# Optimization experiments

Measured on AMD Instinct MI355X. Metric: run time of the kernel, lower is better.

## Reference

```python
import jax, jax.numpy as jnp
import numpy as np

N = 40000      # input points
M = 40000      # output points
E = 500000     # flat neighbor edges (ragged flattened)
F = 32         # input feature channels
C = 64         # output channels
K = 15         # kernel points
EXTENT = 0.6


def _make_kernel_points(k, radius):
    # Deterministic stand-in for load_kernels(): first point fixed at center,
    # remaining points spread inside a ball of the given radius.
    rng = np.random.RandomState(0)
    pts = rng.randn(k, 3).astype(np.float32)
    pts /= np.linalg.norm(pts, axis=1, keepdims=True) + 1e-9
    scale = rng.rand(k, 1).astype(np.float32) ** (1.0 / 3.0)
    pts = pts * scale * radius
    pts[0] = 0.0  # fixed='center'
    return jnp.asarray(pts)


def setup_inputs() -> dict:
    key = jax.random.key(0)
    ks = jax.random.split(key, 6)
    points = jax.random.uniform(ks[0], (N, 3), dtype=jnp.float32)
    features = jax.random.normal(ks[1], (N, F), dtype=jnp.float32)
    output_points = jax.random.uniform(ks[2], (M, 3), dtype=jnp.float32)
    neighbor_indices = jax.random.randint(ks[3], (E,), 0, N, dtype=jnp.int32)
    segment_ids = jnp.sort(jax.random.randint(ks[4], (E,), 0, M, dtype=jnp.int32))
    k_points = _make_kernel_points(K, 1.5 * EXTENT)          # [K,3] constant
    k_values = jax.random.normal(ks[5], (K, F, C), dtype=jnp.float32) * 0.05
    return {
        "points": points,
        "features": features,
        "output_points": output_points,
        "neighbor_indices": neighbor_indices,
        "segment_ids": segment_ids,
        "k_points": k_points,
        "k_values": k_values,
    }


def reference(points, features, output_points, neighbor_indices, segment_ids,
              k_points, k_values):
    # Gather neighbor coords/features and recenter around each output point.
    rel = points[neighbor_indices] - output_points[segment_ids]      # [E,3]
    nbr_feat = features[neighbor_indices]                            # [E,F]

    # Per-kernel-point squared distances and linear influence weights.
    diff = rel[:, None, :] - k_points[None, :, :]                    # [E,K,3]
    sq_dist = jnp.sum(diff * diff, axis=-1)                          # [E,K]
    w = jnp.maximum(1.0 - jnp.sqrt(sq_dist) / EXTENT, 0.0)           # [E,K]

    # Weighted features and ragged segment-sum per output point.
    weighted = w[:, :, None] * nbr_feat[:, None, :]                  # [E,K,F]
    agg = jax.ops.segment_sum(weighted, segment_ids, num_segments=M,
                              indices_are_sorted=True)               # [M,K,F]

    # Batched matmul over kernel points, then sum over kernel points.
    out = jnp.einsum('mkf,kfc->mc', agg, k_values)                   # [M,C]
    return out
```

## Files before the change

kernel.cpp:

```cpp
#include <hip/hip_runtime.h>

typedef __attribute__((ext_vector_type(8))) short bf16x8;
typedef __attribute__((ext_vector_type(8))) _Float16 f16x8;
typedef __attribute__((ext_vector_type(4))) float f32x4;
typedef __attribute__((ext_vector_type(4))) _Float16 f16x4;

#define NPTS   40000
#define MOUT   40000
#define EDG    500000
#define FIN    32
#define COUT   64
#define KP     15
#define KFDIM  (KP * FIN)
#define EXTENT 0.6f

#define FEAT_BLKS  (NPTS * FIN / 1024)
#define PTS_BLKS   ((NPTS + 255) / 256)
#define ROW_BLKS   ((EDG + 255) / 256)
#define PRE_BLKS   (FEAT_BLKS + PTS_BLKS + ROW_BLKS)

__device__ __forceinline__ short f2bf(float x) {
    union { float f; unsigned u; } v; v.f = x;
    unsigned r = (v.u + 0x7fffu + ((v.u >> 16) & 1u)) >> 16;
    return (short)r;
}

__global__ __launch_bounds__(256) void preprocess_all(
    const float* __restrict__ features, _Float16* __restrict__ feat_h,
    const float* __restrict__ pts, float4* __restrict__ p4,
    const int* __restrict__ seg_ids, int* __restrict__ row_start)
{
    const int bid = blockIdx.x;
    if (bid < FEAT_BLKS) {
        const int i = (bid * 256 + threadIdx.x) * 4;
        const float4 v = *(const float4*)(features + i);
        feat_h[i + 0] = (_Float16)v.x;
        feat_h[i + 1] = (_Float16)v.y;
        feat_h[i + 2] = (_Float16)v.z;
        feat_h[i + 3] = (_Float16)v.w;
    } else if (bid < FEAT_BLKS + PTS_BLKS) {
        const int i = (bid - FEAT_BLKS) * 256 + threadIdx.x;
        if (i < NPTS) {
            const float* p = pts + 3 * i;
            p4[i] = make_float4(p[0], p[1], p[2], 0.f);
        }
    } else {
        const int e = (bid - FEAT_BLKS - PTS_BLKS) * 256 + threadIdx.x;
        if (e >= EDG) return;
        const int cur  = seg_ids[e];
        const int prev = (e == 0) ? -1 : seg_ids[e - 1];
        for (int m = prev + 1; m <= cur; ++m) row_start[m] = e;
        if (e == EDG - 1)
            for (int m = cur + 1; m <= MOUT; ++m) row_start[m] = EDG;
    }
}

__global__ __launch_bounds__(256, 8) void kpconv_agg_mfma16(
    const float4* __restrict__ points4,
    const _Float16* __restrict__ feat_h,
    const float* __restrict__ output_points,
    const int*   __restrict__ nbr_idx,
    const int*   __restrict__ row_start,
    const float* __restrict__ k_points,
    _Float16* __restrict__ agg_g)
{
    const int tid  = threadIdx.x;
    const int wave = tid >> 6;
    const int lane = tid & 63;
    const int quad = lane >> 4;
    const int l16  = lane & 15;

    const int m = blockIdx.x * 4 + wave;
    const int e0 = row_start[m], e1 = row_start[m + 1];

    const float ox = output_points[m * 3 + 0];
    const float oy = output_points[m * 3 + 1];
    const float oz = output_points[m * 3 + 2];

    const int myk = l16 < KP ? l16 : 0;
    const float kpx = k_points[myk * 3 + 0];
    const float kpy = k_points[myk * 3 + 1];
    const float kpz = k_points[myk * 3 + 2];
    const float inv_ext = 1.f / EXTENT;

    f32x4 c_lo = {0.f, 0.f, 0.f, 0.f};
    f32x4 c_hi = {0.f, 0.f, 0.f, 0.f};

    for (int es = e0; es < e1; es += 16) {
        const int last = e1 - 1;
        const int ebase = es + quad * 4;

        int nb[4];
        #pragma unroll
        for (int j = 0; j < 4; ++j) {
            const int e = ebase + j;
            nb[j] = nbr_idx[e < e1 ? e : last];
        }

        f16x4 afrag, blo, bhi;
        #pragma unroll
        for (int j = 0; j < 4; ++j) {
            const float4 p = points4[nb[j]];
            const float rx = p.x - ox;
            const float ry = p.y - oy;
            const float rz = p.z - oz;
            const float dx = rx - kpx, dy = ry - kpy, dz = rz - kpz;
            const float d2 = dx * dx + dy * dy + dz * dz;
            float w = 1.f - sqrtf(d2) * inv_ext;
            w = w > 0.f ? w : 0.f;
            if (l16 >= KP || ebase + j >= e1) w = 0.f;
            afrag[j] = (_Float16)w;
        }

        #pragma unroll
        for (int j = 0; j < 4; ++j) {
            const _Float16* fp = feat_h + nb[j] * FIN + l16;
            blo[j] = fp[0];
            bhi[j] = fp[16];
        }

        c_lo = __builtin_amdgcn_mfma_f32_16x16x16f16(afrag, blo, c_lo, 0, 0, 0);
        c_hi = __builtin_amdgcn_mfma_f32_16x16x16f16(afrag, bhi, c_hi, 0, 0, 0);
    }

    _Float16* dst = agg_g + (size_t)m * KFDIM;
    #pragma unroll
    for (int r = 0; r < 4; ++r) {
        const int krow = quad * 4 + r;
        if (krow < KP) {
            dst[krow * FIN + l16]      = (_Float16)c_lo[r];
            dst[krow * FIN + 16 + l16] = (_Float16)c_hi[r];
        }
    }
}

__global__ __launch_bounds__(256, 4) void kpconv_gemm(
    const _Float16* __restrict__ agg_g,
    const float* __restrict__ k_values,
    float* __restrict__ out)
{
    const int tid  = threadIdx.x;
    const int wave = tid >> 6;
    const int lane = tid & 63;
    const int quad = lane >> 4;
    const int l16  = lane & 15;
    const int m0   = blockIdx.x * 32;
    const int bcol = wave * 16 + l16;

    f16x8 bfr[15];
    #pragma unroll
    for (int s = 0; s < 15; ++s) {
        #pragma unroll
        for (int j = 0; j < 8; ++j)
            bfr[s][j] = (_Float16)k_values[(32 * s + quad * 8 + j) * COUT + bcol];
    }

    const _Float16* arow0 = agg_g + (size_t)(m0 + l16) * KFDIM + quad * 8;
    const _Float16* arow1 = arow0 + 16 * KFDIM;

    f32x4 c0 = {0.f, 0.f, 0.f, 0.f};
    f32x4 c1 = {0.f, 0.f, 0.f, 0.f};
    #pragma unroll
    for (int s = 0; s < 15; ++s) {
        const f16x8 a0 = *(const f16x8*)(arow0 + 32 * s);
        const f16x8 a1 = *(const f16x8*)(arow1 + 32 * s);
        c0 = __builtin_amdgcn_mfma_f32_16x16x32_f16(a0, bfr[s], c0, 0, 0, 0);
        c1 = __builtin_amdgcn_mfma_f32_16x16x32_f16(a1, bfr[s], c1, 0, 0, 0);
    }

    #pragma unroll
    for (int r = 0; r < 4; ++r) {
        out[(m0 + quad * 4 + r) * COUT + bcol]      = c0[r];
        out[(m0 + 16 + quad * 4 + r) * COUT + bcol] = c1[r];
    }
}

__global__ __launch_bounds__(256, 4) void kpconv_agg_fallback(
    const float* __restrict__ points,
    const float* __restrict__ features,
    const float* __restrict__ output_points,
    const int*   __restrict__ nbr_idx,
    const int*   __restrict__ seg_ids,
    const float* __restrict__ k_points,
    _Float16* __restrict__ agg_g)
{
    __shared__ int seg_start[5];

    const int tid  = threadIdx.x;
    const int m0   = blockIdx.x * 4;

    if (tid <= 4) {
        const int target = m0 + tid;
        int lo = 0, hi = EDG;
        while (lo < hi) {
            int mid = (lo + hi) >> 1;
            if (seg_ids[mid] < target) lo = mid + 1; else hi = mid;
        }
        seg_start[tid] = lo;
    }
    __syncthreads();

    const int wave = tid >> 6;
    const int lane = tid & 63;
    const int quad = lane >> 4;
    const int l16  = lane & 15;

    const int m = m0 + wave;
    const float ox = output_points[m * 3 + 0];
    const float oy = output_points[m * 3 + 1];
    const float oz = output_points[m * 3 + 2];

    const int myk = l16 < KP ? l16 : 0;
    const float kpx = k_points[myk * 3 + 0];
    const float kpy = k_points[myk * 3 + 1];
    const float kpz = k_points[myk * 3 + 2];
    const float inv_ext = 1.f / EXTENT;

    const int e0 = seg_start[wave], e1 = seg_start[wave + 1];

    f32x4 c_lo = {0.f, 0.f, 0.f, 0.f};
    f32x4 c_hi = {0.f, 0.f, 0.f, 0.f};

    for (int es = e0; es < e1; es += 32) {
        const int last = e1 - 1;
        const int ebase = es + quad * 8;

        int nb[8];
        #pragma unroll
        for (int j = 0; j < 8; ++j) {
            const int e = ebase + j;
            nb[j] = nbr_idx[e < e1 ? e : last];
        }

        bf16x8 afrag, blo, bhi;
        #pragma unroll
        for (int j = 0; j < 8; ++j) {
            const float* pp = points + nb[j] * 3;
            const float rx = pp[0] - ox;
            const float ry = pp[1] - oy;
            const float rz = pp[2] - oz;
            const float dx = rx - kpx, dy = ry - kpy, dz = rz - kpz;
            const float d2 = dx * dx + dy * dy + dz * dz;
            float w = 1.f - sqrtf(d2) * inv_ext;
            w = w > 0.f ? w : 0.f;
            if (l16 >= KP || ebase + j >= e1) w = 0.f;
            afrag[j] = f2bf(w);
        }

        #pragma unroll
        for (int j = 0; j < 8; ++j) {
            const float* fp = features + nb[j] * FIN + l16;
            blo[j] = f2bf(fp[0]);
            bhi[j] = f2bf(fp[16]);
        }

        c_lo = __builtin_amdgcn_mfma_f32_16x16x32_bf16(afrag, blo, c_lo, 0, 0, 0);
        c_hi = __builtin_amdgcn_mfma_f32_16x16x32_bf16(afrag, bhi, c_hi, 0, 0, 0);
    }

    _Float16* dst = agg_g + (size_t)m * KFDIM;
    #pragma unroll
    for (int r = 0; r < 4; ++r) {
        const int krow = quad * 4 + r;
        if (krow < KP) {
            dst[krow * FIN + l16]      = (_Float16)c_lo[r];
            dst[krow * FIN + 16 + l16] = (_Float16)c_hi[r];
        }
    }
}

extern "C" void kernel_launch(void* const* d_in, const int* in_sizes, int n_in,
                              void* d_out, int out_size, void* d_ws, size_t ws_size,
                              hipStream_t stream) {
    const float* points        = (const float*)d_in[0];
    const float* features      = (const float*)d_in[1];
    const float* output_points = (const float*)d_in[2];
    const int*   nbr_idx       = (const int*)d_in[3];
    const int*   seg_ids       = (const int*)d_in[4];
    const float* k_points      = (const float*)d_in[5];
    const float* k_values      = (const float*)d_in[6];
    float* out = (float*)d_out;

    const size_t feat_bytes = (size_t)NPTS * FIN * sizeof(_Float16);
    const size_t pts4_bytes = (size_t)NPTS * sizeof(float4);
    const size_t rs_bytes   = ((size_t)(MOUT + 1) * sizeof(int) + 15) & ~15ul;
    const size_t agg_bytes  = (size_t)MOUT * KFDIM * sizeof(_Float16);
    const size_t full_bytes = feat_bytes + pts4_bytes + rs_bytes + agg_bytes;

    if (ws_size >= full_bytes) {
        char* p = (char*)d_ws;
        _Float16* feat_h    = (_Float16*)p;  p += feat_bytes;
        float4*   points4   = (float4*)p;    p += pts4_bytes;
        int*      row_start = (int*)p;       p += rs_bytes;
        _Float16* agg_g     = (_Float16*)p;

        preprocess_all<<<PRE_BLKS, 256, 0, stream>>>(
            features, feat_h, points, points4, seg_ids, row_start);
        kpconv_agg_mfma16<<<MOUT / 4, 256, 0, stream>>>(
            points4, feat_h, output_points, nbr_idx, row_start, k_points, agg_g);
        kpconv_gemm<<<MOUT / 32, 256, 0, stream>>>(agg_g, k_values, out);
    } else {
        _Float16* agg_g = (_Float16*)d_ws;
        kpconv_agg_fallback<<<MOUT / 4, 256, 0, stream>>>(
            points, features, output_points, nbr_idx, seg_ids, k_points, agg_g);
        kpconv_gemm<<<MOUT / 32, 256, 0, stream>>>(agg_g, k_values, out);
    }
}
```

Measured before the change: 125.4 us.

## Stage per-edge features and weights through LDS with interleaved fp16 layouts

```diff
diff --git a/kernel.cpp b/kernel.cpp
--- a/kernel.cpp
+++ b/kernel.cpp
@@ -4,6 +4,7 @@
 typedef __attribute__((ext_vector_type(8))) _Float16 f16x8;
 typedef __attribute__((ext_vector_type(4))) float f32x4;
 typedef __attribute__((ext_vector_type(4))) _Float16 f16x4;
+typedef __attribute__((ext_vector_type(2))) _Float16 f16x2;
 
 #define NPTS   40000
 #define MOUT   40000
@@ -14,10 +15,16 @@
 #define KFDIM  (KP * FIN)
 #define EXTENT 0.6f
 
+#define FSTRIDE 112
+#define WSTRIDE 40
+#define WAVE_LDS (16 * FSTRIDE + 16 * WSTRIDE)
+
 #define FEAT_BLKS  (NPTS * FIN / 1024)
 #define PTS_BLKS   ((NPTS + 255) / 256)
+#define OP_BLKS    ((MOUT + 255) / 256)
 #define ROW_BLKS   ((EDG + 255) / 256)
-#define PRE_BLKS   (FEAT_BLKS + PTS_BLKS + ROW_BLKS)
+#define WT_BLKS    (KFDIM * COUT / 256)
+#define PRE_BLKS   (FEAT_BLKS + PTS_BLKS + OP_BLKS + ROW_BLKS + WT_BLKS)
 
 __device__ __forceinline__ short f2bf(float x) {
     union { float f; unsigned u; } v; v.f = x;
@@ -26,101 +33,122 @@
 }
 
 __global__ __launch_bounds__(256) void preprocess_all(
-    const float* __restrict__ features, _Float16* __restrict__ feat_h,
+    const float* __restrict__ features, _Float16* __restrict__ feat_i,
     const float* __restrict__ pts, float4* __restrict__ p4,
-    const int* __restrict__ seg_ids, int* __restrict__ row_start)
+    const float* __restrict__ opts, float4* __restrict__ op4,
+    const int* __restrict__ seg_ids, int* __restrict__ row_start,
+    const float* __restrict__ k_values, _Float16* __restrict__ w_t)
 {
     const int bid = blockIdx.x;
     if (bid < FEAT_BLKS) {
-        const int i = (bid * 256 + threadIdx.x) * 4;
-        const float4 v = *(const float4*)(features + i);
-        feat_h[i + 0] = (_Float16)v.x;
-        feat_h[i + 1] = (_Float16)v.y;
-        feat_h[i + 2] = (_Float16)v.z;
-        feat_h[i + 3] = (_Float16)v.w;
+        const int d0 = (bid * 256 + threadIdx.x) * 4;
+        #pragma unroll
+        for (int u = 0; u < 4; ++u) {
+            const int d = d0 + u;
+            const int p = d >> 5, q = d & 31;
+            const int fp = q >> 1, h = q & 1;
+            feat_i[d] = (_Float16)features[p * FIN + fp + 16 * h];
+        }
     } else if (bid < FEAT_BLKS + PTS_BLKS) {
         const int i = (bid - FEAT_BLKS) * 256 + threadIdx.x;
         if (i < NPTS) {
             const float* p = pts + 3 * i;
             p4[i] = make_float4(p[0], p[1], p[2], 0.f);
         }
-    } else {
-        const int e = (bid - FEAT_BLKS - PTS_BLKS) * 256 + threadIdx.x;
+    } else if (bid < FEAT_BLKS + PTS_BLKS + OP_BLKS) {
+        const int i = (bid - FEAT_BLKS - PTS_BLKS) * 256 + threadIdx.x;
+        if (i < MOUT) {
+            const float* p = opts + 3 * i;
+            op4[i] = make_float4(p[0], p[1], p[2], 0.f);
+        }
+    } else if (bid < FEAT_BLKS + PTS_BLKS + OP_BLKS + ROW_BLKS) {
+        const int e = (bid - FEAT_BLKS - PTS_BLKS - OP_BLKS) * 256 + threadIdx.x;
         if (e >= EDG) return;
         const int cur  = seg_ids[e];
         const int prev = (e == 0) ? -1 : seg_ids[e - 1];
         for (int m = prev + 1; m <= cur; ++m) row_start[m] = e;
         if (e == EDG - 1)
             for (int m = cur + 1; m <= MOUT; ++m) row_start[m] = EDG;
-    }
-}
-
-__global__ __launch_bounds__(256, 8) void kpconv_agg_mfma16(
+    } else {
+        const int d = (bid - FEAT_BLKS - PTS_BLKS - OP_BLKS - ROW_BLKS) * 256
+                      + threadIdx.x;
+        const int c = d / KFDIM, r = d % KFDIM;
+        const int k = r >> 5, q = r & 31;
+        const int fp = q >> 1, h = q & 1;
+        w_t[d] = (_Float16)k_values[(k * FIN + fp + 16 * h) * COUT + c];
+    }
+}
+
+__global__ __launch_bounds__(256, 6) void kpconv_agg_edge(
     const float4* __restrict__ points4,
-    const _Float16* __restrict__ feat_h,
-    const float* __restrict__ output_points,
+    const _Float16* __restrict__ feat_i,
+    const float4* __restrict__ op4,
     const int*   __restrict__ nbr_idx,
     const int*   __restrict__ row_start,
     const float* __restrict__ k_points,
     _Float16* __restrict__ agg_g)
 {
+    __shared__ __align__(16) unsigned char smem[4 * WAVE_LDS];
+
     const int tid  = threadIdx.x;
     const int wave = tid >> 6;
     const int lane = tid & 63;
     const int quad = lane >> 4;
     const int l16  = lane & 15;
-
-    const int m = blockIdx.x * 4 + wave;
-    const int e0 = row_start[m], e1 = row_start[m + 1];
-
-    const float ox = output_points[m * 3 + 0];
-    const float oy = output_points[m * 3 + 1];
-    const float oz = output_points[m * 3 + 2];
-
-    const int myk = l16 < KP ? l16 : 0;
-    const float kpx = k_points[myk * 3 + 0];
-    const float kpy = k_points[myk * 3 + 1];
-    const float kpz = k_points[myk * 3 + 2];
+    const int esl  = lane >> 2;
+    const int kg   = lane & 3;
+
+    unsigned char* fbase = smem + wave * WAVE_LDS;
+    unsigned char* wbase = fbase + 16 * FSTRIDE;
+
+    const int m  = blockIdx.x * 4 + wave;
+    const int e0 = row_start[m];
+    const int e1 = row_start[m + 1];
+    const float4 o = op4[m];
+
+    float kx[4], ky[4], kz[4];
+    #pragma unroll
+    for (int t = 0; t < 4; ++t) {
+        const int k  = kg * 4 + t;
+        const int kk = k < KP ? k : 0;
+        kx[t] = k_points[kk * 3 + 0];
+        ky[t] = k_points[kk * 3 + 1];
+        kz[t] = k_points[kk * 3 + 2];
+    }
     const float inv_ext = 1.f / EXTENT;
 
     f32x4 c_lo = {0.f, 0.f, 0.f, 0.f};
     f32x4 c_hi = {0.f, 0.f, 0.f, 0.f};
 
     for (int es = e0; es < e1; es += 16) {
-        const int last = e1 - 1;
-        const int ebase = es + quad * 4;
-
-        int nb[4];
-        #pragma unroll
-        for (int j = 0; j < 4; ++j) {
-            const int e = ebase + j;
-            nb[j] = nbr_idx[e < e1 ? e : last];
-        }
-
-        f16x4 afrag, blo, bhi;
-        #pragma unroll
-        for (int j = 0; j < 4; ++j) {
-            const float4 p = points4[nb[j]];
-            const float rx = p.x - ox;
-            const float ry = p.y - oy;
-            const float rz = p.z - oz;
-            const float dx = rx - kpx, dy = ry - kpy, dz = rz - kpz;
-            const float d2 = dx * dx + dy * dy + dz * dz;
-            float w = 1.f - sqrtf(d2) * inv_ext;
+        const int e  = es + esl;
+        const int nb = nbr_idx[e < e1 ? e : e1 - 1];
+
+        const uint4 fc = *(const uint4*)(feat_i + nb * FIN + kg * 8);
+        *(uint4*)(fbase + esl * FSTRIDE + kg * 16) = fc;
+
+        const float4 p = points4[nb];
+        const float rx = p.x - o.x, ry = p.y - o.y, rz = p.z - o.z;
+        const bool evalid = e < e1;
+        #pragma unroll
+        for (int t = 0; t < 4; ++t) {
+            const float dx = rx - kx[t], dy = ry - ky[t], dz = rz - kz[t];
+            float w = 1.f - sqrtf(dx * dx + dy * dy + dz * dz) * inv_ext;
             w = w > 0.f ? w : 0.f;
-            if (l16 >= KP || ebase + j >= e1) w = 0.f;
-            afrag[j] = (_Float16)w;
-        }
-
-        #pragma unroll
-        for (int j = 0; j < 4; ++j) {
-            const _Float16* fp = feat_h + nb[j] * FIN + l16;
-            blo[j] = fp[0];
-            bhi[j] = fp[16];
-        }
-
-        c_lo = __builtin_amdgcn_mfma_f32_16x16x16f16(afrag, blo, c_lo, 0, 0, 0);
-        c_hi = __builtin_amdgcn_mfma_f32_16x16x16f16(afrag, bhi, c_hi, 0, 0, 0);
+            if (!evalid || (kg * 4 + t) >= KP) w = 0.f;
+            *(_Float16*)(wbase + (kg * 4 + t) * WSTRIDE + esl * 2) = (_Float16)w;
+        }
+
+        const f16x4 af = *(const f16x4*)(wbase + l16 * WSTRIDE + quad * 8);
+        f16x2 w2[4];
+        #pragma unroll
+        for (int j = 0; j < 4; ++j)
+            w2[j] = *(const f16x2*)(fbase + (quad * 4 + j) * FSTRIDE + l16 * 4);
+        const f16x4 blo = {w2[0][0], w2[1][0], w2[2][0], w2[3][0]};
+        const f16x4 bhi = {w2[0][1], w2[1][1], w2[2][1], w2[3][1]};
+
+        c_lo = __builtin_amdgcn_mfma_f32_16x16x16f16(af, blo, c_lo, 0, 0, 0);
+        c_hi = __builtin_amdgcn_mfma_f32_16x16x16f16(af, bhi, c_hi, 0, 0, 0);
     }
 
     _Float16* dst = agg_g + (size_t)m * KFDIM;
@@ -128,15 +156,15 @@
     for (int r = 0; r < 4; ++r) {
         const int krow = quad * 4 + r;
         if (krow < KP) {
-            dst[krow * FIN + l16]      = (_Float16)c_lo[r];
-            dst[krow * FIN + 16 + l16] = (_Float16)c_hi[r];
-        }
-    }
-}
-
-__global__ __launch_bounds__(256, 4) void kpconv_gemm(
+            f16x2 v = {(_Float16)c_lo[r], (_Float16)c_hi[r]};
+            *(f16x2*)(dst + krow * FIN + 2 * l16) = v;
+        }
+    }
+}
+
+__global__ __launch_bounds__(256, 4) void kpconv_gemm_i(
     const _Float16* __restrict__ agg_g,
-    const float* __restrict__ k_values,
+    const _Float16* __restrict__ w_t,
     float* __restrict__ out)
 {
     const int tid  = threadIdx.x;
@@ -148,12 +176,10 @@
     const int bcol = wave * 16 + l16;
 
     f16x8 bfr[15];
-    #pragma unroll
-    for (int s = 0; s < 15; ++s) {
-        #pragma unroll
-        for (int j = 0; j < 8; ++j)
-            bfr[s][j] = (_Float16)k_values[(32 * s + quad * 8 + j) * COUT + bcol];
-    }
+    const _Float16* wrow = w_t + (size_t)bcol * KFDIM + quad * 8;
+    #pragma unroll
+    for (int s = 0; s < 15; ++s)
+        bfr[s] = *(const f16x8*)(wrow + 32 * s);
 
     const _Float16* arow0 = agg_g + (size_t)(m0 + l16) * KFDIM + quad * 8;
     const _Float16* arow1 = arow0 + 16 * KFDIM;
@@ -186,8 +212,8 @@
 {
     __shared__ int seg_start[5];
 
-    const int tid  = threadIdx.x;
-    const int m0   = blockIdx.x * 4;
+    const int tid = threadIdx.x;
+    const int m0  = blockIdx.x * 4;
 
     if (tid <= 4) {
         const int target = m0 + tid;
@@ -269,6 +295,47 @@
     }
 }
 
+__global__ __launch_bounds__(256, 4) void kpconv_gemm_plain(
+    const _Float16* __restrict__ agg_g,
+    const float* __restrict__ k_values,
+    float* __restrict__ out)
+{
+    const int tid  = threadIdx.x;
+    const int wave = tid >> 6;
+    const int lane = tid & 63;
+    const int quad = lane >> 4;
+    const int l16  = lane & 15;
+    const int m0   = blockIdx.x * 32;
+    const int bcol = wave * 16 + l16;
+
+    f16x8 bfr[15];
+    #pragma unroll
+    for (int s = 0; s < 15; ++s) {
+        #pragma unroll
+        for (int j = 0; j < 8; ++j)
+            bfr[s][j] = (_Float16)k_values[(32 * s + quad * 8 + j) * COUT + bcol];
+    }
+
+    const _Float16* arow0 = agg_g + (size_t)(m0 + l16) * KFDIM + quad * 8;
+    const _Float16* arow1 = arow0 + 16 * KFDIM;
+
+    f32x4 c0 = {0.f, 0.f, 0.f, 0.f};
+    f32x4 c1 = {0.f, 0.f, 0.f, 0.f};
+    #pragma unroll
+    for (int s = 0; s < 15; ++s) {
+        const f16x8 a0 = *(const f16x8*)(arow0 + 32 * s);
+        const f16x8 a1 = *(const f16x8*)(arow1 + 32 * s);
+        c0 = __builtin_amdgcn_mfma_f32_16x16x32_f16(a0, bfr[s], c0, 0, 0, 0);
+        c1 = __builtin_amdgcn_mfma_f32_16x16x32_f16(a1, bfr[s], c1, 0, 0, 0);
+    }
+
+    #pragma unroll
+    for (int r = 0; r < 4; ++r) {
+        out[(m0 + quad * 4 + r) * COUT + bcol]      = c0[r];
+        out[(m0 + 16 + quad * 4 + r) * COUT + bcol] = c1[r];
+    }
+}
+
 extern "C" void kernel_launch(void* const* d_in, const int* in_sizes, int n_in,
                               void* d_out, int out_size, void* d_ws, size_t ws_size,
                               hipStream_t stream) {
@@ -283,26 +350,32 @@
 
     const size_t feat_bytes = (size_t)NPTS * FIN * sizeof(_Float16);
     const size_t pts4_bytes = (size_t)NPTS * sizeof(float4);
+    const size_t op4_bytes  = (size_t)MOUT * sizeof(float4);
     const size_t rs_bytes   = ((size_t)(MOUT + 1) * sizeof(int) + 15) & ~15ul;
+    const size_t wt_bytes   = (size_t)KFDIM * COUT * sizeof(_Float16);
     const size_t agg_bytes  = (size_t)MOUT * KFDIM * sizeof(_Float16);
-    const size_t full_bytes = feat_bytes + pts4_bytes + rs_bytes + agg_bytes;
+    const size_t full_bytes = feat_bytes + pts4_bytes + op4_bytes + rs_bytes
+                            + wt_bytes + agg_bytes;
 
     if (ws_size >= full_bytes) {
         char* p = (char*)d_ws;
-        _Float16* feat_h    = (_Float16*)p;  p += feat_bytes;
+        _Float16* feat_i    = (_Float16*)p;  p += feat_bytes;
         float4*   points4   = (float4*)p;    p += pts4_bytes;
+        float4*   op4       = (float4*)p;    p += op4_bytes;
         int*      row_start = (int*)p;       p += rs_bytes;
+        _Float16* w_t       = (_Float16*)p;  p += wt_bytes;
         _Float16* agg_g     = (_Float16*)p;
 
         preprocess_all<<<PRE_BLKS, 256, 0, stream>>>(
-            features, feat_h, points, points4, seg_ids, row_start);
-        kpconv_agg_mfma16<<<MOUT / 4, 256, 0, stream>>>(
-            points4, feat_h, output_points, nbr_idx, row_start, k_points, agg_g);
-        kpconv_gemm<<<MOUT / 32, 256, 0, stream>>>(agg_g, k_values, out);
+            features, feat_i, points, points4, output_points, op4,
+            seg_ids, row_start, k_values, w_t);
+        kpconv_agg_edge<<<MOUT / 4, 256, 0, stream>>>(
+            points4, feat_i, op4, nbr_idx, row_start, k_points, agg_g);
+        kpconv_gemm_i<<<MOUT / 32, 256, 0, stream>>>(agg_g, w_t, out);
     } else {
         _Float16* agg_g = (_Float16*)d_ws;
         kpconv_agg_fallback<<<MOUT / 4, 256, 0, stream>>>(
             points, features, output_points, nbr_idx, seg_ids, k_points, agg_g);
-        kpconv_gemm<<<MOUT / 32, 256, 0, stream>>>(agg_g, k_values, out);
-    }
-}
+        kpconv_gemm_plain<<<MOUT / 32, 256, 0, stream>>>(agg_g, k_values, out);
+    }
+}
```

Result: faster. 117.4 us (-6.4%).
